# Kernel tuning notes

Measured on AMD Instinct MI355X. Metric: run time of the kernel, lower is better.

## Reference

```python
import jax, jax.numpy as jnp
import numpy as np

N = 100000   # nodes
E = 1000000  # edges
G = 128      # graphs in batch
F = 128      # nfeat
H = 64       # nhid
C = 10       # nclass
L = 4        # num_layers
BN_EPS = 1e-5


def setup_inputs() -> dict:
    key = jax.random.key(0)
    ks = jax.random.split(key, 12)
    s = 0.05
    x = jax.random.normal(ks[0], (N, F), jnp.float32)
    ei = jax.random.randint(ks[1], (2, E), 0, N, dtype=jnp.int32)
    ew = jax.random.normal(ks[2], (E,), jnp.float32)  # edge_attr, unused by GIN forward
    batch = jnp.sort(jax.random.randint(ks[3], (N,), 0, G, dtype=jnp.int32))
    W0 = jax.random.normal(ks[4], (F, H), jnp.float32) * s
    b0 = jnp.zeros((H,), jnp.float32)
    convW1 = jax.random.normal(ks[5], (L, H, H), jnp.float32) * s
    convb1 = jnp.zeros((L, H), jnp.float32)
    convg1 = jnp.ones((L, H), jnp.float32)
    convbt1 = jnp.zeros((L, H), jnp.float32)
    convW2 = jax.random.normal(ks[6], (L, H, H), jnp.float32) * s
    convb2 = jnp.zeros((L, H), jnp.float32)
    convg2 = jnp.ones((L, H), jnp.float32)
    convbt2 = jnp.zeros((L, H), jnp.float32)
    Wl1 = jax.random.normal(ks[7], (H, H), jnp.float32) * s
    bl1 = jnp.zeros((H,), jnp.float32)
    Wl2 = jax.random.normal(ks[8], (H, C), jnp.float32) * s
    bl2 = jnp.zeros((C,), jnp.float32)
    return dict(x=x, ei=ei, ew=ew, batch=batch, W0=W0, b0=b0,
                convW1=convW1, convb1=convb1, convg1=convg1, convbt1=convbt1,
                convW2=convW2, convb2=convb2, convg2=convg2, convbt2=convbt2,
                Wl1=Wl1, bl1=bl1, Wl2=Wl2, bl2=bl2)


def _bn(h, g, b):
    # BatchNorm1d in eval mode: running_mean=0, running_var=1
    return h * (g / jnp.sqrt(1.0 + BN_EPS)) + b


def reference(x, ei, ew, batch, W0, b0, convW1, convb1, convg1, convbt1,
              convW2, convb2, convg2, convbt2, Wl1, bl1, Wl2, bl2):
    # linear0 -> (dropout p=0, eval) -> relu
    h = jax.nn.relu(x @ W0 + b0)  # [N, H]
    src, dst = ei[0], ei[1]
    for i in range(L):
        # GINConv, eps=0: mlp((1+0)*x + sum_{j in N(i)} x_j)
        agg = jax.ops.segment_sum(h[src], dst, num_segments=N)  # scatter-add
        z = h + agg
        z = jax.nn.relu(_bn(z @ convW1[i] + convb1[i], convg1[i], convbt1[i]))
        h = jax.nn.relu(_bn(z @ convW2[i] + convb2[i], convg2[i], convbt2[i]))
    h = jax.nn.relu(h @ Wl1 + bl1)
    # global mean pool per graph
    sums = jax.ops.segment_sum(h, batch, num_segments=G)          # [G, H]
    cnt = jax.ops.segment_sum(jnp.ones((N, 1), h.dtype), batch, num_segments=G)
    pooled = sums / jnp.maximum(cnt, 1.0)
    return jax.nn.softmax(pooled @ Wl2 + bl2, axis=1)  # [G, C]
```

## Files before the change

kernel.cpp:

```cpp
#include <hip/hip_runtime.h>
#include <hip/hip_bf16.h>

#define HH 64
#define FF 128
#define CC 10
#define LL 4
#define MAXD 32
#define BN_RSQRT 0.9999950000374997f

typedef __hip_bfloat16 bf16;
using short8 = __attribute__((ext_vector_type(8))) short;
using f32x4  = __attribute__((ext_vector_type(4))) float;
using f32x2  = __attribute__((ext_vector_type(2))) float;

__device__ __forceinline__ float us2f(unsigned short u) {
    return __uint_as_float(((unsigned)u) << 16);
}
__device__ __forceinline__ unsigned short f2bf(float v) {
    unsigned u = __float_as_uint(v);
    return (unsigned short)((u + 0x7FFFu + ((u >> 16) & 1u)) >> 16);
}

#if defined(__has_builtin)
#if __has_builtin(__builtin_amdgcn_cvt_pk_f32_fp8) && __has_builtin(__builtin_amdgcn_cvt_pk_fp8_f32)
#define FP8_HW 1
#endif
#endif

#ifdef FP8_HW
template <bool HIGH>
__device__ __forceinline__ f32x2 fp8_dec2(unsigned w) {
    return __builtin_amdgcn_cvt_pk_f32_fp8((int)w, HIGH);
}
__device__ __forceinline__ unsigned fp8_enc4(float f0, float f1, float f2, float f3) {
    int w = 0;
    w = __builtin_amdgcn_cvt_pk_fp8_f32(f0, f1, w, false);
    w = __builtin_amdgcn_cvt_pk_fp8_f32(f2, f3, w, true);
    return (unsigned)w;
}
#else
__device__ __forceinline__ float fp8_dec1(unsigned b) {
    unsigned s = (b & 0x80u) << 24;
    unsigned em = b & 0x7Fu;
    float mag;
    if (em >= 0x08u) mag = __uint_as_float((((em >> 3) + 120u) << 23) | ((em & 7u) << 20));
    else             mag = (float)em * (1.0f / 512.0f);
    return __uint_as_float(__float_as_uint(mag) | s);
}
template <bool HIGH>
__device__ __forceinline__ f32x2 fp8_dec2(unsigned w) {
    unsigned lo = HIGH ? ((w >> 16) & 0xffu) : (w & 0xffu);
    unsigned hi = HIGH ? ((w >> 24) & 0xffu) : ((w >> 8) & 0xffu);
    f32x2 r; r.x = fp8_dec1(lo); r.y = fp8_dec1(hi); return r;
}
__device__ __forceinline__ unsigned fp8_enc1(float v) {
    unsigned u = __float_as_uint(v);
    unsigned s = (u >> 24) & 0x80u;
    float a = fabsf(v);
    if (a >= 448.0f) return s | 0x7Eu;
    if (a < 0.015625f) {
        int m = (int)rintf(a * 512.0f);
        return s | (unsigned)m;
    }
    int e; float m = frexpf(a, &e);
    int E = e + 6;
    int mant = (int)rintf((m * 2.0f - 1.0f) * 8.0f);
    if (mant == 8) { mant = 0; ++E; }
    if (E > 15) return s | 0x7Eu;
    return s | (unsigned)(E << 3) | (unsigned)mant;
}
__device__ __forceinline__ unsigned fp8_enc4(float f0, float f1, float f2, float f3) {
    return fp8_enc1(f0) | (fp8_enc1(f1) << 8) | (fp8_enc1(f2) << 16) | (fp8_enc1(f3) << 24);
}
#endif

__global__ __launch_bounds__(256) void pack_weights_kernel(
    const float* __restrict__ W0, const float* __restrict__ convW1,
    const float* __restrict__ convW2, const float* __restrict__ Wl1,
    short* __restrict__ wf)
{
    int t = blockIdx.x * 256 + threadIdx.x;
    if (t >= 5632) return;
    const float* W;
    int l, tile, kc, out_idx;
    if (t < 1024) {
        int local = t; int fi = local >> 6; l = local & 63;
        tile = fi >> 2; kc = fi & 3;
        W = W0; out_idx = local;
    } else if (t < 5120) {
        int t2 = t - 1024;
        int m = t2 >> 9;
        int local = t2 & 511;
        int fi = local >> 6; l = local & 63;
        tile = fi >> 1; kc = fi & 1;
        int layer = m >> 1, g = m & 1;
        W = (g ? convW2 : convW1) + (size_t)layer * HH * HH;
        out_idx = 1024 + m * 512 + local;
    } else {
        int local = t - 5120;
        int fi = local >> 6; l = local & 63;
        tile = fi >> 1; kc = fi & 1;
        W = Wl1; out_idx = 5120 + local;
    }
    int k0 = kc * 32 + (l >> 4) * 8;
    int n = tile * 16 + (l & 15);
#pragma unroll
    for (int e = 0; e < 8; ++e)
        wf[out_idx * 8 + e] = (short)f2bf(W[(k0 + e) * HH + n]);
}

__global__ __launch_bounds__(256) void lin0_kernel(
    const float* __restrict__ x, const short8* __restrict__ wf0,
    const float* __restrict__ b0, unsigned char* __restrict__ h, int nrows)
{
    __shared__ __align__(16) short lds_all[4][2048];
    int wave = __builtin_amdgcn_readfirstlane(threadIdx.x >> 6);
    int lane = threadIdx.x & 63;
    char* ldsb = (char*)&lds_all[wave][0];
    int r0 = (blockIdx.x * 4 + wave) * 16;

#pragma unroll
    for (int r = 0; r < 16; ++r) {
        int row = r0 + r;
        float2 xv = make_float2(0.f, 0.f);
        if (row < nrows) xv = *(const float2*)(x + (size_t)row * FF + lane * 2);
        unsigned pk = (unsigned)f2bf(xv.x) | ((unsigned)f2bf(xv.y) << 16);
        *(int*)(ldsb + r * 256 + ((lane * 4) ^ ((r & 7) << 4))) = pk;
    }
    __syncthreads();

    short8 a[4];
#pragma unroll
    for (int kc = 0; kc < 4; ++kc) {
        int rr = lane & 15;
        a[kc] = *(const short8*)(ldsb + rr * 256 + (((kc * 64 + (lane >> 4) * 16)) ^ ((rr & 7) << 4)));
    }
    f32x4 acc[4];
#pragma unroll
    for (int tile = 0; tile < 4; ++tile) {
        acc[tile] = (f32x4){0.f, 0.f, 0.f, 0.f};
#pragma unroll
        for (int kc = 0; kc < 4; ++kc) {
            short8 b = wf0[(tile * 4 + kc) * 64 + lane];
            acc[tile] = __builtin_amdgcn_mfma_f32_16x16x32_bf16(a[kc], b, acc[tile], 0, 0, 0);
        }
    }
    __syncthreads();
#pragma unroll
    for (int tile = 0; tile < 4; ++tile) {
        int col = tile * 16 + (lane & 15);
        float bia = b0[col];
#pragma unroll
        for (int q = 0; q < 4; ++q) {
            int row = (lane >> 4) * 4 + q;
            float v = fmaxf(acc[tile][q] + bia, 0.0f);
            *(short*)(ldsb + row * 256 + ((col * 2) ^ ((row & 7) << 4))) = (short)f2bf(v);
        }
    }
    __syncthreads();
#pragma unroll
    for (int half = 0; half < 2; ++half) {
        int row = (lane >> 3) + half * 8;
        short8 vv = *(const short8*)(ldsb + row * 256 + ((((lane & 7) * 16)) ^ ((row & 7) << 4)));
        int grow = r0 + row;
        if (grow < nrows) {
            unsigned w0 = fp8_enc4(us2f((unsigned short)vv[0]), us2f((unsigned short)vv[1]),
                                   us2f((unsigned short)vv[2]), us2f((unsigned short)vv[3]));
            unsigned w1 = fp8_enc4(us2f((unsigned short)vv[4]), us2f((unsigned short)vv[5]),
                                   us2f((unsigned short)vv[6]), us2f((unsigned short)vv[7]));
            *(uint2*)(h + (size_t)grow * 64 + (lane & 7) * 8) = make_uint2(w0, w1);
        }
    }
}

__global__ __launch_bounds__(256) void hist_kernel(
    const int* __restrict__ dst, int* __restrict__ deg, int nedges)
{
    int e = blockIdx.x * 256 + threadIdx.x;
    if (e < nedges) atomicAdd(&deg[dst[e]], 1);
}

__global__ __launch_bounds__(256) void scan_block_kernel(
    const int* __restrict__ deg, int* __restrict__ rowptr,
    int* __restrict__ partials, int n)
{
    __shared__ int sm[256];
    int tid = threadIdx.x;
    int i = blockIdx.x * 256 + tid;
    int v = (i < n) ? deg[i] : 0;
    sm[tid] = v;
    __syncthreads();
    for (int ofs = 1; ofs < 256; ofs <<= 1) {
        int t = (tid >= ofs) ? sm[tid - ofs] : 0;
        __syncthreads();
        sm[tid] += t;
        __syncthreads();
    }
    if (i < n) rowptr[i] = sm[tid] - v;
    if (tid == 255) partials[blockIdx.x] = sm[255];
}

__global__ __launch_bounds__(256) void scan_partials_kernel(int* partials, int nb)
{
    __shared__ int sm[256];
    __shared__ int carry;
    int tid = threadIdx.x;
    if (tid == 0) carry = 0;
    __syncthreads();
    for (int base = 0; base < nb; base += 256) {
        int i = base + tid;
        int v = (i < nb) ? partials[i] : 0;
        sm[tid] = v;
        __syncthreads();
        for (int ofs = 1; ofs < 256; ofs <<= 1) {
            int t = (tid >= ofs) ? sm[tid - ofs] : 0;
            __syncthreads();
            sm[tid] += t;
            __syncthreads();
        }
        int cbase = carry;
        int tot = sm[255];
        if (i < nb) partials[i] = sm[tid] - v + cbase;
        __syncthreads();
        if (tid == 0) carry = cbase + tot;
        __syncthreads();
    }
}

__global__ __launch_bounds__(256) void add_offsets_kernel(
    int* __restrict__ rowptr, const int* __restrict__ partials, int n)
{
    int i = blockIdx.x * 256 + threadIdx.x;
    if (i < n) rowptr[i] += partials[blockIdx.x];
}

__global__ __launch_bounds__(256) void place_kernel(
    const int* __restrict__ src, const int* __restrict__ dst,
    const int* __restrict__ rowptr, int* __restrict__ deg,
    int* __restrict__ csr, int nedges, int stride)
{
    int t = blockIdx.x * 256 + threadIdx.x;
    int e[4], d[4], slot[4];
    bool ok[4];
#pragma unroll
    for (int i = 0; i < 4; ++i) {
        e[i] = t + i * stride;
        ok[i] = e[i] < nedges;
        d[i] = ok[i] ? dst[e[i]] : 0;
    }
#pragma unroll
    for (int i = 0; i < 4; ++i)
        slot[i] = ok[i] ? atomicAdd(&deg[d[i]], 1) : 0;
#pragma unroll
    for (int i = 0; i < 4; ++i)
        if (ok[i]) csr[rowptr[d[i]] + slot[i]] = src[e[i]];
}

__global__ __launch_bounds__(256) void deg_hist_kernel(
    const int* __restrict__ deg, int* __restrict__ dhist, int n)
{
    __shared__ int lh[64];
    int tid = threadIdx.x;
    if (tid < 64) lh[tid] = 0;
    __syncthreads();
    int i = blockIdx.x * 256 + tid;
    if (i < n) atomicAdd(&lh[min(deg[i], 63)], 1);
    __syncthreads();
    if (tid < 64 && lh[tid]) atomicAdd(&dhist[tid], lh[tid]);
}

__global__ __launch_bounds__(64) void bucket_scan_kernel(
    const int* __restrict__ dhist, int* __restrict__ dcnt)
{
    __shared__ int sm[64];
    int t = threadIdx.x;
    sm[t] = dhist[t];
    __syncthreads();
    int acc = 0;
    for (int k = 0; k < t; ++k) acc += sm[k];
    dcnt[t] = acc;
}

__global__ __launch_bounds__(256) void perm_place_kernel(
    const int* __restrict__ deg, int* __restrict__ dcnt,
    int* __restrict__ perm, int n)
{
    __shared__ int lh[64], lbase[64];
    int tid = threadIdx.x;
    if (tid < 64) lh[tid] = 0;
    __syncthreads();
    int i = blockIdx.x * 256 + tid;
    int b = 0;
    if (i < n) { b = min(deg[i], 63); atomicAdd(&lh[b], 1); }
    __syncthreads();
    if (tid < 64) {
        int cntb = lh[tid];
        if (cntb) lbase[tid] = atomicAdd(&dcnt[tid], cntb);
        lh[tid] = 0;
    }
    __syncthreads();
    if (i < n) {
        int r = atomicAdd(&lh[b], 1);
        perm[lbase[b] + r] = i;
    }
}

template <int FINAL>
__global__ __launch_bounds__(256) void layer_kernel(
    const unsigned char* __restrict__ h, const int* __restrict__ rowptr,
    const int* __restrict__ deg, const int* __restrict__ csr,
    const int* __restrict__ perm,
    const short8* __restrict__ wfG1, const short8* __restrict__ wfG2,
    const float* __restrict__ b1, const float* __restrict__ g1, const float* __restrict__ bt1,
    const float* __restrict__ b2, const float* __restrict__ g2, const float* __restrict__ bt2,
    unsigned char* __restrict__ out, int nrows,
    const short8* __restrict__ wfL1, const float* __restrict__ bl1,
    const int* __restrict__ batch, float* __restrict__ pooled, float* __restrict__ cnt)
{
    __shared__ __align__(16) short lds_all[4][1024];
    __shared__ int idx_tab[4][16][MAXD + 4];
    int wave = __builtin_amdgcn_readfirstlane(threadIdx.x >> 6);
    int lane = threadIdx.x & 63;
    char* ldsb = (char*)&lds_all[wave][0];
    int r0 = (blockIdx.x * 4 + wave) * 16;

    int s16[16], c16[16], maxc = 0;
#pragma unroll
    for (int r = 0; r < 16; ++r) {
        int gi = r0 + r;
        int pr = nrows;
        int sv = 0, cv = 0;
        if (gi < nrows) {
            pr = perm ? perm[gi] : gi;
            sv = rowptr[pr]; cv = deg[pr];
        }
        pr = __builtin_amdgcn_readfirstlane(pr);
        s16[r] = __builtin_amdgcn_readfirstlane(sv);
        c16[r] = __builtin_amdgcn_readfirstlane(cv);
        maxc = max(maxc, c16[r]);
        int idxv = nrows;
        if (lane < c16[r]) idxv = csr[s16[r] + lane];
        idxv = min(max(idxv, 0), nrows) << 6;
        if (lane < MAXD) idx_tab[wave][r][lane] = idxv;
        if (lane == 0) idx_tab[wave][r][MAXD] = pr << 6;
    }

    int selrow = lane >> 4;
    int fq4 = (lane & 15) * 4;
    int fq8 = fq4 * 2;

    float zg[4][4];
#pragma unroll
    for (int g = 0; g < 4; ++g) {
        int bo = idx_tab[wave][g * 4 + selrow][MAXD];
        unsigned w = *(const unsigned*)(h + bo + fq4);
        f32x2 lo = fp8_dec2<false>(w), hi = fp8_dec2<true>(w);
        zg[g][0] = lo.x; zg[g][1] = lo.y; zg[g][2] = hi.x; zg[g][3] = hi.y;
    }

    int jm = min(maxc, MAXD);
    for (int j0 = 0; j0 < jm; j0 += 4) {
        unsigned w[4][4];
#pragma unroll
        for (int jj = 0; jj < 4; ++jj) {
            int jcl = min(j0 + jj, MAXD - 1);
#pragma unroll
            for (int g = 0; g < 4; ++g) {
                int bo = idx_tab[wave][g * 4 + selrow][jcl];
                w[jj][g] = *(const unsigned*)(h + bo + fq4);
            }
        }
#pragma unroll
        for (int jj = 0; jj < 4; ++jj)
#pragma unroll
            for (int g = 0; g < 4; ++g) {
                f32x2 lo = fp8_dec2<false>(w[jj][g]), hi = fp8_dec2<true>(w[jj][g]);
                zg[g][0] += lo.x; zg[g][1] += lo.y; zg[g][2] += hi.x; zg[g][3] += hi.y;
            }
    }
    if (maxc > MAXD) {
#pragma unroll
        for (int g = 0; g < 4; ++g) {
#pragma unroll
            for (int q = 0; q < 4; ++q) {
                int r = g * 4 + q;
                for (int j = MAXD; j < c16[r]; ++j) {
                    int sn = csr[s16[r] + j];
                    sn = min(max(sn, 0), nrows - 1);
                    unsigned w = *(const unsigned*)(h + ((size_t)sn << 6) + fq4);
                    f32x2 lo = fp8_dec2<false>(w), hi = fp8_dec2<true>(w);
                    bool mine = (selrow == q);
                    zg[g][0] += mine ? lo.x : 0.f;
                    zg[g][1] += mine ? lo.y : 0.f;
                    zg[g][2] += mine ? hi.x : 0.f;
                    zg[g][3] += mine ? hi.y : 0.f;
                }
            }
        }
    }

#pragma unroll
    for (int g = 0; g < 4; ++g) {
        int row = g * 4 + selrow;
        unsigned d0 = (unsigned)f2bf(zg[g][0]) | ((unsigned)f2bf(zg[g][1]) << 16);
        unsigned d1 = (unsigned)f2bf(zg[g][2]) | ((unsigned)f2bf(zg[g][3]) << 16);
        int off = (row * 128 + fq8) ^ ((row & 7) << 4);
        *(uint2*)(ldsb + off) = make_uint2(d0, d1);
    }
    __syncthreads();

    short8 a0, a1;
    f32x4 acc[4];
    {
        int rr = lane & 15;
        a0 = *(const short8*)(ldsb + rr * 128 + (((lane >> 4) * 16) ^ ((rr & 7) << 4)));
        a1 = *(const short8*)(ldsb + rr * 128 + ((64 + (lane >> 4) * 16) ^ ((rr & 7) << 4)));
    }
#pragma unroll
    for (int tile = 0; tile < 4; ++tile) {
        acc[tile] = (f32x4){0.f, 0.f, 0.f, 0.f};
        acc[tile] = __builtin_amdgcn_mfma_f32_16x16x32_bf16(a0, wfG1[(tile * 2 + 0) * 64 + lane], acc[tile], 0, 0, 0);
        acc[tile] = __builtin_amdgcn_mfma_f32_16x16x32_bf16(a1, wfG1[(tile * 2 + 1) * 64 + lane], acc[tile], 0, 0, 0);
    }
    __syncthreads();
#pragma unroll
    for (int tile = 0; tile < 4; ++tile) {
        int col = tile * 16 + (lane & 15);
        float sc = g1[col] * BN_RSQRT;
        float sh = fmaf(b1[col], sc, bt1[col]);
#pragma unroll
        for (int q = 0; q < 4; ++q) {
            int row = (lane >> 4) * 4 + q;
            float v = fmaxf(fmaf(acc[tile][q], sc, sh), 0.0f);
            *(short*)(ldsb + row * 128 + ((col * 2) ^ ((row & 7) << 4))) = (short)f2bf(v);
        }
    }
    __syncthreads();

    {
        int rr = lane & 15;
        a0 = *(const short8*)(ldsb + rr * 128 + (((lane >> 4) * 16) ^ ((rr & 7) << 4)));
        a1 = *(const short8*)(ldsb + rr * 128 + ((64 + (lane >> 4) * 16) ^ ((rr & 7) << 4)));
    }
#pragma unroll
    for (int tile = 0; tile < 4; ++tile) {
        acc[tile] = (f32x4){0.f, 0.f, 0.f, 0.f};
        acc[tile] = __builtin_amdgcn_mfma_f32_16x16x32_bf16(a0, wfG2[(tile * 2 + 0) * 64 + lane], acc[tile], 0, 0, 0);
        acc[tile] = __builtin_amdgcn_mfma_f32_16x16x32_bf16(a1, wfG2[(tile * 2 + 1) * 64 + lane], acc[tile], 0, 0, 0);
    }
    __syncthreads();
#pragma unroll
    for (int tile = 0; tile < 4; ++tile) {
        int col = tile * 16 + (lane & 15);
        float sc = g2[col] * BN_RSQRT;
        float sh = fmaf(b2[col], sc, bt2[col]);
#pragma unroll
        for (int q = 0; q < 4; ++q) {
            int row = (lane >> 4) * 4 + q;
            float v = fmaxf(fmaf(acc[tile][q], sc, sh), 0.0f);
            *(short*)(ldsb + row * 128 + ((col * 2) ^ ((row & 7) << 4))) = (short)f2bf(v);
        }
    }
    __syncthreads();

    if (FINAL == 0) {
#pragma unroll
        for (int half = 0; half < 2; ++half) {
            int row = (lane >> 3) + half * 8;
            short8 vv = *(const short8*)(ldsb + row * 128 + ((((lane & 7) * 16)) ^ ((row & 7) << 4)));
            int ro = idx_tab[wave][row][MAXD];
            if (ro < (nrows << 6)) {
                unsigned w0 = fp8_enc4(us2f((unsigned short)vv[0]), us2f((unsigned short)vv[1]),
                                       us2f((unsigned short)vv[2]), us2f((unsigned short)vv[3]));
                unsigned w1 = fp8_enc4(us2f((unsigned short)vv[4]), us2f((unsigned short)vv[5]),
                                       us2f((unsigned short)vv[6]), us2f((unsigned short)vv[7]));
                *(uint2*)(out + ro + (lane & 7) * 8) = make_uint2(w0, w1);
            }
        }
    } else {
        {
            int rr = lane & 15;
            a0 = *(const short8*)(ldsb + rr * 128 + (((lane >> 4) * 16) ^ ((rr & 7) << 4)));
            a1 = *(const short8*)(ldsb + rr * 128 + ((64 + (lane >> 4) * 16) ^ ((rr & 7) << 4)));
        }
#pragma unroll
        for (int tile = 0; tile < 4; ++tile) {
            acc[tile] = (f32x4){0.f, 0.f, 0.f, 0.f};
            acc[tile] = __builtin_amdgcn_mfma_f32_16x16x32_bf16(a0, wfL1[(tile * 2 + 0) * 64 + lane], acc[tile], 0, 0, 0);
            acc[tile] = __builtin_amdgcn_mfma_f32_16x16x32_bf16(a1, wfL1[(tile * 2 + 1) * 64 + lane], acc[tile], 0, 0, 0);
        }
        __syncthreads();
#pragma unroll
        for (int tile = 0; tile < 4; ++tile) {
            int col = tile * 16 + (lane & 15);
            float bia = bl1[col];
#pragma unroll
            for (int q = 0; q < 4; ++q) {
                int row = (lane >> 4) * 4 + q;
                float v = fmaxf(acc[tile][q] + bia, 0.0f);
                *(short*)(ldsb + row * 128 + ((col * 2) ^ ((row & 7) << 4))) = (short)f2bf(v);
            }
        }
        __syncthreads();
        float pacc = 0.0f;
        int curg = -1, rc = 0;
        for (int r = 0; r < 16; ++r) {
            int row = r0 + r;
            if (row >= nrows) break;
            float v = us2f(*(const unsigned short*)(ldsb + r * 128 + ((lane * 2) ^ ((r & 7) << 4))));
            int g = batch[row];
            if (g != curg) {
                if (curg >= 0) {
                    atomicAdd(&pooled[curg * HH + lane], pacc);
                    if (lane == 0) atomicAdd(&cnt[curg], (float)rc);
                }
                curg = g; pacc = v; rc = 1;
            } else { pacc += v; rc += 1; }
        }
        if (curg >= 0) {
            atomicAdd(&pooled[curg * HH + lane], pacc);
            if (lane == 0) atomicAdd(&cnt[curg], (float)rc);
        }
    }
}

__global__ __launch_bounds__(64) void head_kernel(
    const float* __restrict__ pooled, const float* __restrict__ cnt,
    const float* __restrict__ Wl2, const float* __restrict__ bl2,
    float* __restrict__ out, int ngraphs)
{
    int gidx = blockIdx.x * 64 + threadIdx.x;
    if (gidx >= ngraphs) return;
    float logits[CC];
#pragma unroll
    for (int c = 0; c < CC; ++c) logits[c] = bl2[c];
    float inv_n = 1.0f / fmaxf(cnt[gidx], 1.0f);
    for (int k = 0; k < HH; ++k) {
        float p = pooled[gidx * HH + k] * inv_n;
#pragma unroll
        for (int c = 0; c < CC; ++c) logits[c] = fmaf(p, Wl2[k * CC + c], logits[c]);
    }
    float m = logits[0];
#pragma unroll
    for (int c = 1; c < CC; ++c) m = fmaxf(m, logits[c]);
    float ssum = 0.0f;
#pragma unroll
    for (int c = 0; c < CC; ++c) { logits[c] = __expf(logits[c] - m); ssum += logits[c]; }
    float inv = 1.0f / ssum;
#pragma unroll
    for (int c = 0; c < CC; ++c) out[gidx * CC + c] = logits[c] * inv;
}

extern "C" void kernel_launch(void* const* d_in, const int* in_sizes, int n_in,
                              void* d_out, int out_size, void* d_ws, size_t ws_size,
                              hipStream_t stream) {
    const float* x      = (const float*)d_in[0];
    const int*   ei     = (const int*)  d_in[1];
    const int*   batch  = (const int*)  d_in[3];
    const float* W0     = (const float*)d_in[4];
    const float* b0     = (const float*)d_in[5];
    const float* convW1 = (const float*)d_in[6];
    const float* convb1 = (const float*)d_in[7];
    const float* convg1 = (const float*)d_in[8];
    const float* convbt1= (const float*)d_in[9];
    const float* convW2 = (const float*)d_in[10];
    const float* convb2 = (const float*)d_in[11];
    const float* convg2 = (const float*)d_in[12];
    const float* convbt2= (const float*)d_in[13];
    const float* Wl1    = (const float*)d_in[14];
    const float* bl1    = (const float*)d_in[15];
    const float* Wl2    = (const float*)d_in[16];
    const float* bl2    = (const float*)d_in[17];

    const int N = in_sizes[0] / FF;
    const int E = in_sizes[1] / 2;
    const int G = out_size / CC;

    const int* src = ei;
    const int* dst = ei + E;

    size_t off = 0;
    auto take = [&](size_t bytes) { size_t p = off; off = (off + bytes + 255) & ~255ULL; return p; };
    int NB = (N + 255) / 256;
    int EB = (E + 255) / 256;
    size_t o_rowptr = take((size_t)N * 4);
    size_t o_deg    = take((size_t)N * 4);
    size_t o_csr    = take((size_t)(E > NB ? E : NB) * 4 + 512);
    size_t o_perm   = take((size_t)N * 4);
    size_t o_dhist  = take(64 * 4);
    size_t o_dcnt   = take(64 * 4);
    size_t o_pooled = take((size_t)G * HH * 4);
    size_t o_cnt    = take((size_t)G * 4);
    size_t o_wfrag  = take((size_t)5632 * 8 * 2);
    size_t o_hA     = take((size_t)(N + 1) * 64);
    size_t o_hB     = take((size_t)(N + 1) * 64);

    char* base = (char*)d_ws;
    int*    rowptr = (int*)(base + o_rowptr);
    int*    deg    = (int*)(base + o_deg);
    int*    csr    = (int*)(base + o_csr);
    int*    perm   = (int*)(base + o_perm);
    int*    dhist  = (int*)(base + o_dhist);
    int*    dcnt   = (int*)(base + o_dcnt);
    float*  pooled = (float*)(base + o_pooled);
    float*  cnt    = (float*)(base + o_cnt);
    short*  wfrag  = (short*)(base + o_wfrag);
    short8* wf8    = (short8*)wfrag;
    unsigned char* hA = (unsigned char*)(base + o_hA);
    unsigned char* hB = (unsigned char*)(base + o_hB);

    int tile_blocks = (N + 63) / 64;

    pack_weights_kernel<<<22, 256, 0, stream>>>(W0, convW1, convW2, Wl1, wfrag);

    (void)hipMemsetAsync(deg, 0, (size_t)N * sizeof(int), stream);
    hist_kernel<<<EB, 256, 0, stream>>>(dst, deg, E);
    scan_block_kernel<<<NB, 256, 0, stream>>>(deg, rowptr, csr , N);
    scan_partials_kernel<<<1, 256, 0, stream>>>(csr, NB);
    add_offsets_kernel<<<NB, 256, 0, stream>>>(rowptr, csr, N);
    (void)hipMemsetAsync(deg, 0, (size_t)N * sizeof(int), stream);
    {
        int stride = ((E + 3) / 4 + 255) & ~255;
        place_kernel<<<stride / 256, 256, 0, stream>>>(src, dst, rowptr, deg, csr, E, stride);
    }

    (void)hipMemsetAsync(dhist, 0, 64 * sizeof(int), stream);
    deg_hist_kernel<<<NB, 256, 0, stream>>>(deg, dhist, N);
    bucket_scan_kernel<<<1, 64, 0, stream>>>(dhist, dcnt);
    perm_place_kernel<<<NB, 256, 0, stream>>>(deg, dcnt, perm, N);

    (void)hipMemsetAsync(hA + (size_t)N * 64, 0, 64, stream);
    (void)hipMemsetAsync(hB + (size_t)N * 64, 0, 64, stream);

    lin0_kernel<<<tile_blocks, 256, 0, stream>>>(x, wf8, b0, hA, N);

    (void)hipMemsetAsync(pooled, 0, (size_t)G * HH * sizeof(float), stream);
    (void)hipMemsetAsync(cnt, 0, (size_t)G * sizeof(float), stream);

    const unsigned char* hin = hA; unsigned char* hout = hB;
    const short8* wfL1 = wf8 + 5120;
    for (int l = 0; l < LL; ++l) {
        const short8* wfG1 = wf8 + 1024 + (size_t)(l * 2 + 0) * 512;
        const short8* wfG2 = wf8 + 1024 + (size_t)(l * 2 + 1) * 512;
        if (l < LL - 1) {
            layer_kernel<0><<<tile_blocks, 256, 0, stream>>>(
                hin, rowptr, deg, csr, perm, wfG1, wfG2,
                convb1 + l * HH, convg1 + l * HH, convbt1 + l * HH,
                convb2 + l * HH, convg2 + l * HH, convbt2 + l * HH,
                hout, N, nullptr, nullptr, nullptr, nullptr, nullptr);
        } else {
            layer_kernel<1><<<tile_blocks, 256, 0, stream>>>(
                hin, rowptr, deg, csr, nullptr, wfG1, wfG2,
                convb1 + l * HH, convg1 + l * HH, convbt1 + l * HH,
                convb2 + l * HH, convg2 + l * HH, convbt2 + l * HH,
                nullptr, N, wfL1, bl1, batch, pooled, cnt);
        }
        unsigned char* tswap = (unsigned char*)hin; hin = hout; hout = tswap;
    }

    head_kernel<<<(G + 63) / 64, 64, 0, stream>>>(pooled, cnt, Wl2, bl2, (float*)d_out, G);
}
```

Measured before the change: 327.1 us.

## Two-pass CSR build: bin edges by 128-node buckets before placing

Replaces the single scatter pass that placed each edge directly into CSR with two passes. The first bins packed (dst low bits, src) words into per-128-node bucket regions using per-bucket atomic cursors. The second pass has one block per bucket place edges into the CSR with per-node atomics, which keeps atomics and writes within a small address window. This aims to cut random global atomic and scatter traffic, at the cost of an extra kernel, an extra E-sized buffer and an extra round trip over the edges. Src is packed into 25 bits, which assumes N < 2^25.

```diff
diff --git a/kernel.cpp b/kernel.cpp
--- a/kernel.cpp
+++ b/kernel.cpp
@@ -234,26 +234,53 @@
     if (i < n) rowptr[i] += partials[blockIdx.x];
 }
 
-__global__ __launch_bounds__(256) void place_kernel(
+__global__ __launch_bounds__(256) void bcur_init_kernel(
+    const int* __restrict__ rowptr, int* __restrict__ bcur, int nbuck)
+{
+    int b = blockIdx.x * 256 + threadIdx.x;
+    if (b < nbuck) bcur[b] = rowptr[b << 7];
+}
+
+__global__ __launch_bounds__(256) void bin_kernel(
     const int* __restrict__ src, const int* __restrict__ dst,
-    const int* __restrict__ rowptr, int* __restrict__ deg,
-    int* __restrict__ csr, int nedges, int stride)
+    int* __restrict__ bcur, unsigned* __restrict__ ebuf, int nedges, int stride)
 {
     int t = blockIdx.x * 256 + threadIdx.x;
-    int e[4], d[4], slot[4];
+    int e[4], d[4], pos[4];
+    unsigned pk[4];
     bool ok[4];
 #pragma unroll
     for (int i = 0; i < 4; ++i) {
         e[i] = t + i * stride;
         ok[i] = e[i] < nedges;
         d[i] = ok[i] ? dst[e[i]] : 0;
+        int s = ok[i] ? src[e[i]] : 0;
+        pk[i] = ((unsigned)(d[i] & 127) << 25) | (unsigned)s;
     }
 #pragma unroll
     for (int i = 0; i < 4; ++i)
-        slot[i] = ok[i] ? atomicAdd(&deg[d[i]], 1) : 0;
+        pos[i] = ok[i] ? atomicAdd(&bcur[d[i] >> 7], 1) : 0;
 #pragma unroll
     for (int i = 0; i < 4; ++i)
-        if (ok[i]) csr[rowptr[d[i]] + slot[i]] = src[e[i]];
+        if (ok[i]) ebuf[pos[i]] = pk[i];
+}
+
+__global__ __launch_bounds__(256) void place2_kernel(
+    const unsigned* __restrict__ ebuf, const int* __restrict__ rowptr,
+    int* __restrict__ deg, int* __restrict__ csr, int n, int nedges)
+{
+    int b = blockIdx.x;
+    int base = rowptr[b << 7];
+    int hin = (b + 1) << 7;
+    int end = (hin < n) ? rowptr[hin] : nedges;
+    int nb0 = b << 7;
+    for (int i = base + threadIdx.x; i < end; i += 256) {
+        unsigned pk = ebuf[i];
+        int s = (int)(pk & 0x1FFFFFFu);
+        int d = nb0 + (int)(pk >> 25);
+        int slot = atomicAdd(&deg[d], 1);
+        csr[rowptr[d] + slot] = s;
+    }
 }
 
 __global__ __launch_bounds__(256) void deg_hist_kernel(
@@ -583,9 +610,12 @@
     auto take = [&](size_t bytes) { size_t p = off; off = (off + bytes + 255) & ~255ULL; return p; };
     int NB = (N + 255) / 256;
     int EB = (E + 255) / 256;
+    int nbuck = (N + 127) >> 7;
     size_t o_rowptr = take((size_t)N * 4);
     size_t o_deg    = take((size_t)N * 4);
     size_t o_csr    = take((size_t)(E > NB ? E : NB) * 4 + 512);
+    size_t o_ebuf   = take((size_t)E * 4);
+    size_t o_bcur   = take((size_t)nbuck * 4);
     size_t o_perm   = take((size_t)N * 4);
     size_t o_dhist  = take(64 * 4);
     size_t o_dcnt   = take(64 * 4);
@@ -596,16 +626,18 @@
     size_t o_hB     = take((size_t)(N + 1) * 64);
 
     char* base = (char*)d_ws;
-    int*    rowptr = (int*)(base + o_rowptr);
-    int*    deg    = (int*)(base + o_deg);
-    int*    csr    = (int*)(base + o_csr);
-    int*    perm   = (int*)(base + o_perm);
-    int*    dhist  = (int*)(base + o_dhist);
-    int*    dcnt   = (int*)(base + o_dcnt);
-    float*  pooled = (float*)(base + o_pooled);
-    float*  cnt    = (float*)(base + o_cnt);
-    short*  wfrag  = (short*)(base + o_wfrag);
-    short8* wf8    = (short8*)wfrag;
+    int*      rowptr = (int*)(base + o_rowptr);
+    int*      deg    = (int*)(base + o_deg);
+    int*      csr    = (int*)(base + o_csr);
+    unsigned* ebuf   = (unsigned*)(base + o_ebuf);
+    int*      bcur   = (int*)(base + o_bcur);
+    int*      perm   = (int*)(base + o_perm);
+    int*      dhist  = (int*)(base + o_dhist);
+    int*      dcnt   = (int*)(base + o_dcnt);
+    float*    pooled = (float*)(base + o_pooled);
+    float*    cnt    = (float*)(base + o_cnt);
+    short*    wfrag  = (short*)(base + o_wfrag);
+    short8*   wf8    = (short8*)wfrag;
     unsigned char* hA = (unsigned char*)(base + o_hA);
     unsigned char* hB = (unsigned char*)(base + o_hB);
 
@@ -618,11 +650,14 @@
     scan_block_kernel<<<NB, 256, 0, stream>>>(deg, rowptr, csr , N);
     scan_partials_kernel<<<1, 256, 0, stream>>>(csr, NB);
     add_offsets_kernel<<<NB, 256, 0, stream>>>(rowptr, csr, N);
+
+    bcur_init_kernel<<<(nbuck + 255) / 256, 256, 0, stream>>>(rowptr, bcur, nbuck);
     (void)hipMemsetAsync(deg, 0, (size_t)N * sizeof(int), stream);
     {
         int stride = ((E + 3) / 4 + 255) & ~255;
-        place_kernel<<<stride / 256, 256, 0, stream>>>(src, dst, rowptr, deg, csr, E, stride);
-    }
+        bin_kernel<<<stride / 256, 256, 0, stream>>>(src, dst, bcur, ebuf, E, stride);
+    }
+    place2_kernel<<<nbuck, 256, 0, stream>>>(ebuf, rowptr, deg, csr, N, E);
 
     (void)hipMemsetAsync(dhist, 0, 64 * sizeof(int), stream);
     deg_hist_kernel<<<NB, 256, 0, stream>>>(deg, dhist, N);
```

Result: slower. 540.3 us (+65.2%).
